# Performance work log

Hardware: AMD Instinct MI355X
Metric: run time of the kernel (lower is better)

Reference implementation:

```python
import jax, jax.numpy as jnp
import numpy as np

H_MIN = -1.0
H_MAX = 1.0
B_SAT = 1.0
N = 256          # Preisach mesh size (n x n)
M = 4000         # number of applied-field time steps


def setup_inputs() -> dict:
    key = jax.random.key(0)
    k1, k2 = jax.random.split(key)
    # applied magnetic field history, spanning [h_min, h_max]
    h_data = jax.random.uniform(k1, (M,), dtype=jnp.float32, minval=-1.0, maxval=1.0)
    # raw (pre-softplus) hysteresis density vector, length n(n+1)/2
    raw = jax.random.normal(k2, (N * (N + 1) // 2,), dtype=jnp.float32)
    return {"h_data": h_data, "raw_hyst_density_vector": raw}


def reference(h_data, raw_hyst_density_vector):
    n = N
    dt = h_data.dtype
    x = jnp.linspace(0.0, 1.0, n, dtype=dt)
    # 'xy' indexing: xx varies along columns (beta thresholds), yy along rows (alpha thresholds)
    xx, yy = jnp.meshgrid(x, x)
    tril_mask = jnp.tril(jnp.ones((n, n), dtype=dt))

    # normalize_h
    h_norm = (h_data - H_MIN) / (H_MAX - H_MIN)
    hs = jnp.concatenate([jnp.full((1,), -H_MIN, dtype=dt), h_norm])  # (M+1,)
    # torch indexing hs[i-1] wraps to hs[-1] at i=0 -> roll by 1
    hp = jnp.roll(hs, 1)

    init = -jnp.ones((n, n), dtype=dt)

    def step(state, hh):
        h, p = hh
        swept_up = jnp.where(yy >= h, state, jnp.asarray(1.0, dt))    # sweep up: flip below alpha threshold
        swept_dn = jnp.where(xx <= h, state, jnp.asarray(-1.0, dt))   # sweep left: flip above beta threshold
        s = jnp.where(h > p, swept_up, jnp.where(h < p, swept_dn, state))
        s = s * tril_mask  # torch.tril each step
        return s, s

    _, states = jax.lax.scan(step, init, (hs, hp))  # (M+1, n, n)

    dens_vec = jax.nn.softplus(raw_hyst_density_vector)
    ti, tj = jnp.tril_indices(n)
    dens = jnp.zeros((n, n), dtype=dens_vec.dtype).at[ti, tj].set(dens_vec)
    a = B_SAT / jnp.sum(dens)

    # b[i] = sum(dens * states[i+1])
    b = jnp.einsum('tij,ij->t', states[1:], dens)
    return b * a
```

## Files before the change

kernel.cpp:

```cpp
#include <hip/hip_runtime.h>

#define NN 256
#define TT 16

__device__ __forceinline__ float softplus_f(float x) {
    if (x > 20.0f) return x;
    return log1pf(expf(x));
}

__global__ void __launch_bounds__(256)
kA(const float* __restrict__ h_g, const float* __restrict__ raw, int M, int G,
   float* __restrict__ PrefT, float* __restrict__ RowTot,
   int* __restrict__ steps_g, unsigned int* __restrict__ UDt)
{
    int b = blockIdx.x, tid = threadIdx.x;
    if (b < NN) {
        __shared__ float wsum[4];
        float x = 0.0f;
        if (tid <= b) x = softplus_f(raw[b * (b + 1) / 2 + tid]);
        int lane = tid & 63, wv = tid >> 6;
        #pragma unroll
        for (int off = 1; off <= 32; off <<= 1) {
            float y = __shfl_up(x, off, 64);
            if (lane >= off) x += y;
        }
        if (lane == 63) wsum[wv] = x;
        __syncthreads();
        float add = 0.0f;
        if (wv > 0) add += wsum[0];
        if (wv > 1) add += wsum[1];
        if (wv > 2) add += wsum[2];
        x += add;
        PrefT[(tid + 1) * NN + b] = x;
        if (tid == 0)      PrefT[b] = 0.0f;
        if (tid == NN - 1) RowTot[b] = x;
    } else {
        __shared__ float xs[NN];
        __shared__ float hh[TT + 1];
        __shared__ int   dd[TT + 1];
        int c  = b - NN;
        int t0 = c * TT;
        int Tb = min(TT, M - t0);
        xs[tid] = (float)((double)tid / 255.0);
        __syncthreads();
        if (tid < Tb) {
            int tau = t0 + 1 + tid;
            float cur  = (h_g[tau - 1] + 1.0f) * 0.5f;
            float prev = (tau == 1) ? 1.0f : (h_g[tau - 2] + 1.0f) * 0.5f;
            int d = (cur > prev) ? 2 : ((cur < prev) ? 0 : 1);
            int lo = 0, hi = NN;
            while (lo < hi) { int m = (lo + hi) >> 1; if (xs[m] < cur) lo = m + 1; else hi = m; }
            int ih = lo;
            lo = 0; hi = NN;
            while (lo < hi) { int m = (lo + hi) >> 1; if (xs[m] <= cur) lo = m + 1; else hi = m; }
            int jh = lo;
            hh[1 + tid] = cur;
            dd[1 + tid] = d - 1;
            steps_g[tau] = d | (ih << 2) | (jh << 11);
        }
        __syncthreads();
        float xi = xs[tid];
        int Ue = 0, De = 0;
        for (int k = 1; k <= Tb; ++k) {
            float hv = hh[k]; int d = dd[k];
            if (d > 0 && hv > xi) Ue = t0 + k + 1;
            if (d < 0 && hv < xi) De = t0 + k + 1;
        }
        UDt[c * NN + tid] = (unsigned)Ue | ((unsigned)De << 16);
    }
}

__global__ void __launch_bounds__(256)
kM(const float* __restrict__ h_g, const unsigned int* __restrict__ UDt,
   unsigned int* __restrict__ PrefUD, int M, int G)
{
    int tid = threadIdx.x;
    float hsM = (h_g[M - 1] + 1.0f) * 0.5f;
    unsigned u = (hsM < 1.0f && tid < NN - 1) ? 1u : 0u;
    unsigned d = 0u;
    const unsigned int* p = UDt + tid;
    unsigned int* q = PrefUD + tid;
    int k = 0;
    for (; k + 8 <= G; k += 8) {
        unsigned vv[8];
        #pragma unroll
        for (int uu = 0; uu < 8; ++uu) vv[uu] = p[(k + uu) * NN];
        #pragma unroll
        for (int uu = 0; uu < 8; ++uu) {
            q[(k + uu) * NN] = u | (d << 16);
            unsigned ue = vv[uu] & 0xFFFFu, de = vv[uu] >> 16;
            if (ue > u) u = ue;
            if (de > d) d = de;
        }
    }
    for (; k < G; ++k) {
        unsigned v = p[k * NN];
        q[k * NN] = u | (d << 16);
        unsigned ue = v & 0xFFFFu, de = v >> 16;
        if (ue > u) u = ue;
        if (de > d) d = de;
    }
}

__global__ void __launch_bounds__(256)
kB(const int* __restrict__ steps_g, const unsigned int* __restrict__ PrefUD,
   const float* __restrict__ PrefT, const float* __restrict__ RowTot,
   float* __restrict__ out, int M)
{
    __shared__ int   rec_s[TT + 1];
    __shared__ int   Dv[NN];
    __shared__ float red[4 * (TT + 2)];
    __shared__ float tot[TT + 2];
    int b = blockIdx.x, tid = threadIdx.x;
    int t0 = b * TT;
    int Tb = min(TT, M - t0);

    if (tid < TT) rec_s[1 + tid] = (tid < Tb) ? steps_g[t0 + 1 + tid] : 0;
    float RT = RowTot[tid];

    unsigned v = PrefUD[b * NN + tid];
    int Ue = (int)(v & 0xFFFFu);
    Dv[tid] = (int)(v >> 16);
    __syncthreads();

    float pk[TT + 1];
    #pragma unroll
    for (int kk = 1; kk <= TT; ++kk) {
        int jh = (rec_s[kk] >> 11) & 0x1FF;
        pk[kk] = PrefT[jh * NN + tid];
    }

    int lo = 0, hi = NN;
    while (lo < hi) { int m = (lo + hi) >> 1; if (Dv[m] < Ue) lo = m + 1; else hi = m; }
    int c = min(lo, tid + 1);
    float w = 2.0f * PrefT[c * NN + tid] - RT;

    float vals[TT + 2];
    vals[0] = RT; vals[1] = w;
    int cc = c; float ww = w;
    #pragma unroll
    for (int kk = 1; kk <= TT; ++kk) {
        float dl = 0.0f;
        if (kk <= Tb) {
            int rec = rec_s[kk];
            int d = rec & 3;
            if (d == 2) {
                int ih = (rec >> 2) & 0x1FF;
                if (tid < ih) { dl = RT - ww; ww = RT; cc = tid + 1; }
            } else if (d == 0) {
                int jh = (rec >> 11) & 0x1FF;
                if (cc > jh) { float wn = 2.0f * pk[kk] - RT; dl = wn - ww; ww = wn; cc = jh; }
            }
        }
        vals[1 + kk] = dl;
    }

    #pragma unroll
    for (int q = 0; q < TT + 2; ++q)
        for (int off = 32; off; off >>= 1)
            vals[q] += __shfl_down(vals[q], off, 64);
    int lane = tid & 63, wv = tid >> 6;
    if (lane == 0) {
        #pragma unroll
        for (int q = 0; q < TT + 2; ++q) red[wv * (TT + 2) + q] = vals[q];
    }
    __syncthreads();
    if (tid < TT + 2)
        tot[tid] = red[tid] + red[(TT + 2) + tid] + red[2 * (TT + 2) + tid] + red[3 * (TT + 2) + tid];
    __syncthreads();
    if (tid < TT) {
        float x = tot[2 + tid];
        #pragma unroll
        for (int off = 1; off < TT; off <<= 1) {
            float y = __shfl_up(x, off, 64);
            if (tid >= off) x += y;
        }
        if (tid < Tb) out[t0 + tid] = (tot[1] + x) * (1.0f / tot[0]);
    }
}

extern "C" void kernel_launch(void* const* d_in, const int* in_sizes, int n_in,
                              void* d_out, int out_size, void* d_ws, size_t ws_size,
                              hipStream_t stream) {
    const float* h   = (const float*)d_in[0];
    const float* raw = (const float*)d_in[1];
    float* out = (float*)d_out;
    int M = in_sizes[0];
    int G = (M + TT - 1) / TT;

    char* ws = (char*)d_ws;
    size_t off = 0;
    auto take = [&](size_t bytes) { size_t cur = off; off = (off + bytes + 255) & ~(size_t)255; return cur; };
    float*        PrefT  = (float*)(ws + take((size_t)(NN + 1) * NN * 4));
    float*        RowTot = (float*)(ws + take((size_t)NN * 4));
    int*          steps  = (int*)(ws + take((size_t)(M + 1) * 4));
    unsigned int* UDt    = (unsigned int*)(ws + take((size_t)G * NN * 4));
    unsigned int* PrefUD = (unsigned int*)(ws + take((size_t)G * NN * 4));

    kA<<<NN + G, 256, 0, stream>>>(h, raw, M, G, PrefT, RowTot, steps, UDt);
    kM<<<1, 256, 0, stream>>>(h, UDt, PrefUD, M, G);
    kB<<<G, 256, 0, stream>>>(steps, PrefUD, PrefT, RowTot, out, M);
}
```

Measured before the change: 77.20 us.

## Fuse three kernels into one cooperative kernel with grid sync and per-block prefix max

Merges the setup, serial prefix-max, and evaluation kernels into a single cooperative launch that uses a grid-wide barrier. The single-block serial scan over chunks is removed: each evaluation block now recomputes its own prefix max by reading every earlier chunk's UDt entries. This cuts launch overhead and the serial single-block bottleneck, but adds redundant reads that grow quadratically with chunk count, plus a grid sync cost. If the cooperative launch fails, it falls back to two launches.

```diff
diff --git a/kernel.cpp b/kernel.cpp
--- a/kernel.cpp
+++ b/kernel.cpp
@@ -1,4 +1,7 @@
 #include <hip/hip_runtime.h>
+#include <hip/hip_cooperative_groups.h>
+
+namespace cg = cooperative_groups;
 
 #define NN 256
 #define TT 16
@@ -8,119 +11,116 @@
     return log1pf(expf(x));
 }
 
-__global__ void __launch_bounds__(256)
-kA(const float* __restrict__ h_g, const float* __restrict__ raw, int M, int G,
-   float* __restrict__ PrefT, float* __restrict__ RowTot,
-   int* __restrict__ steps_g, unsigned int* __restrict__ UDt)
+__global__ void __launch_bounds__(256, 2)
+kMain(const float* __restrict__ h_g, const float* __restrict__ raw,
+      float* __restrict__ out, int M, int G,
+      float* __restrict__ PrefT, float* __restrict__ RowTot,
+      int* __restrict__ steps_g, unsigned int* __restrict__ UDt, int mode)
 {
-    int b = blockIdx.x, tid = threadIdx.x;
-    if (b < NN) {
-        __shared__ float wsum[4];
-        float x = 0.0f;
-        if (tid <= b) x = softplus_f(raw[b * (b + 1) / 2 + tid]);
-        int lane = tid & 63, wv = tid >> 6;
-        #pragma unroll
-        for (int off = 1; off <= 32; off <<= 1) {
-            float y = __shfl_up(x, off, 64);
-            if (lane >= off) x += y;
-        }
-        if (lane == 63) wsum[wv] = x;
-        __syncthreads();
-        float add = 0.0f;
-        if (wv > 0) add += wsum[0];
-        if (wv > 1) add += wsum[1];
-        if (wv > 2) add += wsum[2];
-        x += add;
-        PrefT[(tid + 1) * NN + b] = x;
-        if (tid == 0)      PrefT[b] = 0.0f;
-        if (tid == NN - 1) RowTot[b] = x;
-    } else {
-        __shared__ float xs[NN];
-        __shared__ float hh[TT + 1];
-        __shared__ int   dd[TT + 1];
-        int c  = b - NN;
-        int t0 = c * TT;
-        int Tb = min(TT, M - t0);
-        xs[tid] = (float)((double)tid / 255.0);
-        __syncthreads();
-        if (tid < Tb) {
-            int tau = t0 + 1 + tid;
-            float cur  = (h_g[tau - 1] + 1.0f) * 0.5f;
-            float prev = (tau == 1) ? 1.0f : (h_g[tau - 2] + 1.0f) * 0.5f;
-            int d = (cur > prev) ? 2 : ((cur < prev) ? 0 : 1);
-            int lo = 0, hi = NN;
-            while (lo < hi) { int m = (lo + hi) >> 1; if (xs[m] < cur) lo = m + 1; else hi = m; }
-            int ih = lo;
-            lo = 0; hi = NN;
-            while (lo < hi) { int m = (lo + hi) >> 1; if (xs[m] <= cur) lo = m + 1; else hi = m; }
-            int jh = lo;
-            hh[1 + tid] = cur;
-            dd[1 + tid] = d - 1;
-            steps_g[tau] = d | (ih << 2) | (jh << 11);
-        }
-        __syncthreads();
-        float xi = xs[tid];
-        int Ue = 0, De = 0;
-        for (int k = 1; k <= Tb; ++k) {
-            float hv = hh[k]; int d = dd[k];
-            if (d > 0 && hv > xi) Ue = t0 + k + 1;
-            if (d < 0 && hv < xi) De = t0 + k + 1;
-        }
-        UDt[c * NN + tid] = (unsigned)Ue | ((unsigned)De << 16);
-    }
-}
-
-__global__ void __launch_bounds__(256)
-kM(const float* __restrict__ h_g, const unsigned int* __restrict__ UDt,
-   unsigned int* __restrict__ PrefUD, int M, int G)
-{
-    int tid = threadIdx.x;
-    float hsM = (h_g[M - 1] + 1.0f) * 0.5f;
-    unsigned u = (hsM < 1.0f && tid < NN - 1) ? 1u : 0u;
-    unsigned d = 0u;
-    const unsigned int* p = UDt + tid;
-    unsigned int* q = PrefUD + tid;
-    int k = 0;
-    for (; k + 8 <= G; k += 8) {
-        unsigned vv[8];
-        #pragma unroll
-        for (int uu = 0; uu < 8; ++uu) vv[uu] = p[(k + uu) * NN];
-        #pragma unroll
-        for (int uu = 0; uu < 8; ++uu) {
-            q[(k + uu) * NN] = u | (d << 16);
-            unsigned ue = vv[uu] & 0xFFFFu, de = vv[uu] >> 16;
-            if (ue > u) u = ue;
-            if (de > d) d = de;
-        }
-    }
-    for (; k < G; ++k) {
-        unsigned v = p[k * NN];
-        q[k * NN] = u | (d << 16);
-        unsigned ue = v & 0xFFFFu, de = v >> 16;
-        if (ue > u) u = ue;
-        if (de > d) d = de;
-    }
-}
-
-__global__ void __launch_bounds__(256)
-kB(const int* __restrict__ steps_g, const unsigned int* __restrict__ PrefUD,
-   const float* __restrict__ PrefT, const float* __restrict__ RowTot,
-   float* __restrict__ out, int M)
-{
+    __shared__ float xs[NN];
+    __shared__ float hh[TT + 1];
+    __shared__ int   dd[TT + 1];
     __shared__ int   rec_s[TT + 1];
     __shared__ int   Dv[NN];
     __shared__ float red[4 * (TT + 2)];
     __shared__ float tot[TT + 2];
-    int b = blockIdx.x, tid = threadIdx.x;
-    int t0 = b * TT;
+    __shared__ float wsum[4];
+
+    const int b = blockIdx.x, tid = threadIdx.x;
+    const bool fused = (mode == 0);
+
+    if (mode != 2) {
+        if (b < NN) {
+            float x = 0.0f;
+            if (tid <= b) x = softplus_f(raw[b * (b + 1) / 2 + tid]);
+            int lane = tid & 63, wv = tid >> 6;
+            #pragma unroll
+            for (int off = 1; off <= 32; off <<= 1) {
+                float y = __shfl_up(x, off, 64);
+                if (lane >= off) x += y;
+            }
+            if (lane == 63) wsum[wv] = x;
+            __syncthreads();
+            float add = 0.0f;
+            if (wv > 0) add += wsum[0];
+            if (wv > 1) add += wsum[1];
+            if (wv > 2) add += wsum[2];
+            x += add;
+            PrefT[(tid + 1) * NN + b] = x;
+            if (tid == 0)      PrefT[b] = 0.0f;
+            if (tid == NN - 1) RowTot[b] = x;
+        } else {
+            int c  = b - NN;
+            int t0 = c * TT;
+            int Tb = min(TT, M - t0);
+            xs[tid] = (float)((double)tid / 255.0);
+            if (tid < TT) rec_s[1 + tid] = 0;
+            __syncthreads();
+            if (tid < Tb) {
+                int tau = t0 + 1 + tid;
+                float cur  = (h_g[tau - 1] + 1.0f) * 0.5f;
+                float prev = (tau == 1) ? 1.0f : (h_g[tau - 2] + 1.0f) * 0.5f;
+                int d = (cur > prev) ? 2 : ((cur < prev) ? 0 : 1);
+                int lo = 0, hi = NN;
+                while (lo < hi) { int m = (lo + hi) >> 1; if (xs[m] < cur) lo = m + 1; else hi = m; }
+                int ih = lo;
+                lo = 0; hi = NN;
+                while (lo < hi) { int m = (lo + hi) >> 1; if (xs[m] <= cur) lo = m + 1; else hi = m; }
+                int jh = lo;
+                hh[1 + tid] = cur;
+                dd[1 + tid] = d - 1;
+                int rec = d | (ih << 2) | (jh << 11);
+                rec_s[1 + tid] = rec;
+                if (mode == 1) steps_g[tau] = rec;
+            }
+            __syncthreads();
+            float xi = xs[tid];
+            int Ue = 0, De = 0;
+            for (int k = 1; k <= Tb; ++k) {
+                float hv = hh[k]; int d = dd[k];
+                if (d > 0 && hv > xi) Ue = t0 + k + 1;
+                if (d < 0 && hv < xi) De = t0 + k + 1;
+            }
+            UDt[c * NN + tid] = (unsigned)Ue | ((unsigned)De << 16);
+        }
+    }
+
+    if (fused) cg::this_grid().sync();
+    if (mode == 1) return;
+
+    int c;
+    if (fused) { if (b < NN) return; c = b - NN; }
+    else       { c = b; }
+    int t0 = c * TT;
     int Tb = min(TT, M - t0);
 
-    if (tid < TT) rec_s[1 + tid] = (tid < Tb) ? steps_g[t0 + 1 + tid] : 0;
+    if (mode == 2) {
+        if (tid < TT) rec_s[1 + tid] = (tid < Tb) ? steps_g[t0 + 1 + tid] : 0;
+        __syncthreads();
+    }
+
     float RT = RowTot[tid];
 
-    unsigned v = PrefUD[b * NN + tid];
-    int Ue = (int)(v & 0xFFFFu);
-    Dv[tid] = (int)(v >> 16);
+    float hsM = (h_g[M - 1] + 1.0f) * 0.5f;
+    unsigned uM = (hsM < 1.0f && tid < NN - 1) ? 1u : 0u;
+    unsigned dM = 0u;
+    const unsigned int* p = UDt + tid;
+    for (int k = 0; k < c; k += 32) {
+        unsigned vv[32];
+        #pragma unroll
+        for (int u = 0; u < 32; ++u) {
+            int idx = k + u; if (idx >= c) idx = c - 1;
+            vv[u] = p[idx * NN];
+        }
+        #pragma unroll
+        for (int u = 0; u < 32; ++u) {
+            unsigned ue = vv[u] & 0xFFFFu, de = vv[u] >> 16;
+            if (ue > uM) uM = ue;
+            if (de > dM) dM = de;
+        }
+    }
+    int Ue = (int)uM;
+    Dv[tid] = (int)dM;
     __syncthreads();
 
     float pk[TT + 1];
@@ -132,12 +132,12 @@
 
     int lo = 0, hi = NN;
     while (lo < hi) { int m = (lo + hi) >> 1; if (Dv[m] < Ue) lo = m + 1; else hi = m; }
-    int c = min(lo, tid + 1);
-    float w = 2.0f * PrefT[c * NN + tid] - RT;
+    int cix = min(lo, tid + 1);
+    float w = 2.0f * PrefT[cix * NN + tid] - RT;
 
     float vals[TT + 2];
     vals[0] = RT; vals[1] = w;
-    int cc = c; float ww = w;
+    int cc = cix; float ww = w;
     #pragma unroll
     for (int kk = 1; kk <= TT; ++kk) {
         float dl = 0.0f;
@@ -195,9 +195,16 @@
     float*        RowTot = (float*)(ws + take((size_t)NN * 4));
     int*          steps  = (int*)(ws + take((size_t)(M + 1) * 4));
     unsigned int* UDt    = (unsigned int*)(ws + take((size_t)G * NN * 4));
-    unsigned int* PrefUD = (unsigned int*)(ws + take((size_t)G * NN * 4));
-
-    kA<<<NN + G, 256, 0, stream>>>(h, raw, M, G, PrefT, RowTot, steps, UDt);
-    kM<<<1, 256, 0, stream>>>(h, UDt, PrefUD, M, G);
-    kB<<<G, 256, 0, stream>>>(steps, PrefUD, PrefT, RowTot, out, M);
+
+    int mode0 = 0;
+    void* args[] = { (void*)&h, (void*)&raw, (void*)&out, (void*)&M, (void*)&G,
+                     (void*)&PrefT, (void*)&RowTot, (void*)&steps, (void*)&UDt,
+                     (void*)&mode0 };
+    hipError_t e = hipLaunchCooperativeKernel((const void*)kMain, dim3(NN + G), dim3(256),
+                                              args, 0, stream);
+    if (e != hipSuccess) {
+        (void)hipGetLastError();
+        kMain<<<NN + G, 256, 0, stream>>>(h, raw, out, M, G, PrefT, RowTot, steps, UDt, 1);
+        kMain<<<G,      256, 0, stream>>>(h, raw, out, M, G, PrefT, RowTot, steps, UDt, 2);
+    }
 }
```

After: 144.9 us. +87.7%, slower.
